# Kernel tuning notes

Measured on AMD Instinct MI355X. Metric: run time of the kernel, lower is better.

## Reference

```python
import jax, jax.numpy as jnp
import numpy as np

HEADS = 8
GROUPS = 8
EPS = 1e-5

def setup_inputs() -> dict:
    key = jax.random.key(0)
    ks = jax.random.split(key, 12)
    B, C, S = 2, 256, 16
    x = jax.random.normal(ks[0], (B, C, S, S, S), dtype=jnp.float32)
    std = 1.0 / np.sqrt(C)
    def lin(k):
        kw, kb = jax.random.split(k)
        W = jax.random.uniform(kw, (C, C), jnp.float32, -std, std)
        b = jax.random.uniform(kb, (C,), jnp.float32, -std, std)
        return W, b
    Wq, bq = lin(ks[1])
    Wk, bk = lin(ks[2])
    Wv, bv = lin(ks[3])
    Wo, bo = lin(ks[4])
    gamma = jnp.ones((C,), jnp.float32)
    beta = jnp.zeros((C,), jnp.float32)
    return {"x": x, "gamma": gamma, "beta": beta, "Wq": Wq, "bq": bq,
            "Wk": Wk, "bk": bk, "Wv": Wv, "bv": bv, "Wo": Wo, "bo": bo}

def _group_norm(x, gamma, beta):
    B, C = x.shape[0], x.shape[1]
    xg = x.reshape(B, GROUPS, -1)  # [B, G, (C/G)*D*H*W]
    mu = xg.mean(axis=-1, keepdims=True)
    var = xg.var(axis=-1, keepdims=True)
    xg = (xg - mu) * jax.lax.rsqrt(var + EPS)
    xn = xg.reshape(x.shape)
    return xn * gamma[None, :, None, None, None] + beta[None, :, None, None, None]

def _conv1x1(x, W, b):
    # 1x1x1 Conv3d == channel-mixing linear: [B,C,D,H,W] x [O,C]
    return jnp.einsum('bcdhw,oc->bodhw', x, W) + b[None, :, None, None, None]

def reference(x, gamma, beta, Wq, bq, Wk, bk, Wv, bv, Wo, bo):
    B, C, D, H, W = x.shape
    hd = C // HEADS
    N = D * H * W
    xn = _group_norm(x, gamma, beta)
    Q = _conv1x1(xn, Wq, bq).reshape(B, HEADS, hd, N)
    K = _conv1x1(xn, Wk, bk).reshape(B, HEADS, hd, N)
    V = _conv1x1(xn, Wv, bv).reshape(B, HEADS, hd, N)
    scale = jnp.sqrt(jnp.asarray(hd, x.dtype))
    attn = jnp.einsum('bhdn,bhdm->bhnm', Q, K) / scale
    attn = jax.nn.softmax(attn, axis=-1)
    out = jnp.einsum('bhnm,bhdm->bhdn', attn, V).reshape(B, C, D, H, W)
    out = _conv1x1(out, Wo, bo)
    return x + out
```

## Files before the change

### kernel.cpp

```cpp
#include <hip/hip_runtime.h>

typedef unsigned short us;
typedef unsigned int uns;
typedef __attribute__((ext_vector_type(8))) short short8;
typedef __attribute__((ext_vector_type(4))) float floatx4;
typedef __attribute__((ext_vector_type(16))) float floatx16;
typedef __attribute__((ext_vector_type(4))) uns unsx4;

__device__ __forceinline__ us f2b(float f) {
    union { float f; unsigned u; } x; x.f = f;
    unsigned r = x.u + 0x7fffu + ((x.u >> 16) & 1u);
    return (us)(r >> 16);
}
__device__ __forceinline__ uns fbits(float f) {
    union { float f; unsigned u; } x; x.f = f; return x.u;
}
__device__ __forceinline__ uns pk2(float hi, float lo) {
    return __builtin_amdgcn_perm(fbits(hi) + 0x8000u, fbits(lo) + 0x8000u, 0x07060302u);
}
__device__ __forceinline__ uns pk2t(float hi, float lo) {
    return __builtin_amdgcn_perm(fbits(hi), fbits(lo), 0x07060302u);
}
__device__ __forceinline__ float ex2(float x) {
    return __builtin_amdgcn_exp2f(x);
}

#define C_DIM 256
#define N_DIM 4096
#define CN (C_DIM * N_DIM)
#define CSC (0.17677669529663687f * 1.4426950408889634f)

__global__ __launch_bounds__(256) void k_part_prep(
        const float* __restrict__ x, float* __restrict__ part,
        const float* __restrict__ Wq, const float* __restrict__ Wk,
        const float* __restrict__ Wv, const float* __restrict__ Wo,
        const float* __restrict__ bq, const float* __restrict__ bk,
        const float* __restrict__ bv, const float* __restrict__ bo,
        us* __restrict__ Wb, float* __restrict__ bst) {
    const int t = threadIdx.x;
    if (blockIdx.y == 16) {
        const int xb = blockIdx.x;
#pragma unroll
        for (int e = 0; e < 4; ++e) {
            int id = e * 16384 + xb * 256 + t;
            Wb[id]          = f2b(Wq[id] * CSC);
            Wb[65536 + id]  = f2b(Wk[id]);
            Wb[131072 + id] = f2b(Wv[id]);
            Wb[196608 + id] = f2b(Wo[id]);
        }
        if (xb == 0) {
            bst[t]       = bq[t] * CSC;
            bst[256 + t] = bk[t];
            bst[512 + t] = bv[t];
            bst[768 + t] = bo[t];
        }
        return;
    }
    const int bg = blockIdx.y, sl = blockIdx.x;
    const float* base = x + (size_t)bg * 131072 + (size_t)sl * 2048 + t * 8;
    float4 a = *(const float4*)base;
    float4 b = *(const float4*)(base + 4);
    float s  = a.x + a.y + a.z + a.w + b.x + b.y + b.z + b.w;
    float ss = a.x*a.x + a.y*a.y + a.z*a.z + a.w*a.w
             + b.x*b.x + b.y*b.y + b.z*b.z + b.w*b.w;
    __shared__ float r1[256], r2[256];
    r1[t] = s; r2[t] = ss;
    __syncthreads();
    for (int off = 128; off > 0; off >>= 1) {
        if (t < off) { r1[t] += r1[t + off]; r2[t] += r2[t + off]; }
        __syncthreads();
    }
    if (t == 0) {
        part[(bg * 64 + sl) * 2]     = r1[0];
        part[(bg * 64 + sl) * 2 + 1] = r2[0];
    }
}

__global__ __launch_bounds__(256) void k_gn_normT(const float* __restrict__ x,
                                                  const float* __restrict__ gamma,
                                                  const float* __restrict__ beta,
                                                  const float* __restrict__ part,
                                                  us* __restrict__ XT) {
    const int t = threadIdx.x, g = blockIdx.y, z = blockIdx.z;
    const int nb = blockIdx.x & 15, c8 = blockIdx.x >> 4;
    const int bg = z * 8 + g;
    __shared__ float scs[32], offs[32], mv[2];
    if (t < 64) {
        float s  = part[(bg * 64 + t) * 2];
        float ss = part[(bg * 64 + t) * 2 + 1];
#pragma unroll
        for (int off = 1; off < 64; off <<= 1) {
            s  += __shfl_xor(s, off, 64);
            ss += __shfl_xor(ss, off, 64);
        }
        if (t == 0) {
            const float inv = 1.f / 131072.f;
            float mean = s * inv;
            float var  = ss * inv - mean * mean;
            mv[0] = mean; mv[1] = rsqrtf(var + 1e-5f);
        }
    }
    __syncthreads();
    if (t < 32) {
        float sc = mv[1] * gamma[g * 32 + t];
        scs[t]  = sc;
        offs[t] = beta[g * 32 + t] - mv[0] * sc;
    }
    __syncthreads();
    const int n = nb * 256 + t;
    const float* xp = x + ((size_t)z * 256 + g * 32) * N_DIM + n;
    us* op = XT + ((size_t)z * N_DIM + n) * 256 + g * 32;
    short8 o;
#pragma unroll
    for (int i = 0; i < 8; ++i) {
        int c = c8 * 8 + i;
        float v = xp[(size_t)c * N_DIM];
        o[i] = (short)f2b(v * scs[c] + offs[c]);
    }
    *(short8*)(op + c8 * 8) = o;
}

__global__ __launch_bounds__(256) void k_qkv(const us* __restrict__ W,
                                             const float* __restrict__ bias,
                                             const us* __restrict__ XT,
                                             us* __restrict__ QT,
                                             us* __restrict__ KTg,
                                             us* __restrict__ Vb) {
    const int t = threadIdx.x;
    const int n0 = blockIdx.x * 64, m0 = blockIdx.y * 64, z = blockIdx.z;
    const int l = t & 63, w = t >> 6, l15 = l & 15, quad = l >> 4;
    const int wm = m0 + (w >> 1) * 32, wn = n0 + (w & 1) * 32;
    const us* Ap = W + (size_t)(wm + l15) * 256 + quad * 8;
    const us* Bp = XT + ((size_t)z * N_DIM + wn + l15) * 256 + quad * 8;

    floatx4 acc[2][2] = {};
#pragma unroll
    for (int k0 = 0; k0 < 256; k0 += 32) {
        short8 a0 = *(const short8*)(Ap + k0);
        short8 a1 = *(const short8*)(Ap + k0 + 16 * 256);
        short8 b0 = *(const short8*)(Bp + k0);
        short8 b1 = *(const short8*)(Bp + k0 + 16 * 256);
        acc[0][0] = __builtin_amdgcn_mfma_f32_16x16x32_bf16(a0, b0, acc[0][0], 0, 0, 0);
        acc[0][1] = __builtin_amdgcn_mfma_f32_16x16x32_bf16(a0, b1, acc[0][1], 0, 0, 0);
        acc[1][0] = __builtin_amdgcn_mfma_f32_16x16x32_bf16(a1, b0, acc[1][0], 0, 0, 0);
        acc[1][1] = __builtin_amdgcn_mfma_f32_16x16x32_bf16(a1, b1, acc[1][1], 0, 0, 0);
    }

    if (blockIdx.y < 8) {
        us* Dst = (blockIdx.y < 4) ? QT : KTg;
        const int h = (wm >> 5) & 7, bh = z * 8 + h;
#pragma unroll
        for (int mt = 0; mt < 2; ++mt) {
            const int d0 = mt * 16 + quad * 4;
            float b0v = bias[wm + mt * 16 + quad * 4 + 0];
            float b1v = bias[wm + mt * 16 + quad * 4 + 1];
            float b2v = bias[wm + mt * 16 + quad * 4 + 2];
            float b3v = bias[wm + mt * 16 + quad * 4 + 3];
#pragma unroll
            for (int nt = 0; nt < 2; ++nt) {
                int col = wn + nt * 16 + l15;
                uint2 pw;
                pw.x = pk2(acc[mt][nt][1] + b1v, acc[mt][nt][0] + b0v);
                pw.y = pk2(acc[mt][nt][3] + b3v, acc[mt][nt][2] + b2v);
                *(uint2*)(Dst + ((size_t)bh * N_DIM + col) * 32 + d0) = pw;
            }
        }
    } else {
#pragma unroll
        for (int mt = 0; mt < 2; ++mt)
#pragma unroll
            for (int nt = 0; nt < 2; ++nt)
#pragma unroll
                for (int r = 0; r < 4; ++r) {
                    int row = wm + mt * 16 + quad * 4 + r;
                    int col = wn + nt * 16 + l15;
                    Vb[((size_t)z * 256 + (row - 512)) * N_DIM + col] =
                        f2b(acc[mt][nt][r] + bias[row]);
                }
    }
}

__device__ __forceinline__ floatx16 mfma32(short8 a, short8 b, floatx16 c) {
    return __builtin_amdgcn_mfma_f32_32x32x16_bf16(a, b, c, 0, 0, 0);
}
__device__ __forceinline__ void mkfrag(const floatx16& s, short8& p1, short8& p2) {
    uns d0 = pk2t(ex2(s[1]),  ex2(s[0]));
    uns d1 = pk2t(ex2(s[3]),  ex2(s[2]));
    uns d2 = pk2t(ex2(s[5]),  ex2(s[4]));
    uns d3 = pk2t(ex2(s[7]),  ex2(s[6]));
    uns d4 = pk2t(ex2(s[9]),  ex2(s[8]));
    uns d5 = pk2t(ex2(s[11]), ex2(s[10]));
    uns d6 = pk2t(ex2(s[13]), ex2(s[12]));
    uns d7 = pk2t(ex2(s[15]), ex2(s[14]));
    asm volatile("v_permlane32_swap_b32 %0, %1" : "+v"(d0), "+v"(d2));
    asm volatile("v_permlane32_swap_b32 %0, %1" : "+v"(d1), "+v"(d3));
    asm volatile("v_permlane32_swap_b32 %0, %1" : "+v"(d4), "+v"(d6));
    asm volatile("v_permlane32_swap_b32 %0, %1" : "+v"(d5), "+v"(d7));
    unsx4 u1 = {d0, d1, d2, d3};
    unsx4 u2 = {d4, d5, d6, d7};
    p1 = __builtin_bit_cast(short8, u1);
    p2 = __builtin_bit_cast(short8, u2);
}

__global__ __launch_bounds__(512, 4) void k_attn(const us* __restrict__ QT,
                                                 const us* __restrict__ KTg,
                                                 const us* __restrict__ Vb,
                                                 us* __restrict__ AOT) {
    __shared__ __attribute__((aligned(16))) us SM[16384];
    us* Kbase = SM;
    us* Vbase = SM + 8192;
    const int t = threadIdx.x;
    const int l = t & 63, w = t >> 6, hf = l >> 5, k31 = l & 31;
    const int sw = w & 3, kh = w >> 2;
    const int bh = blockIdx.y, z = bh >> 3, hd = bh & 7;
    const us* KTp = KTg + (size_t)bh * N_DIM * 32;
    const us* Vp  = Vb  + ((size_t)z * 256 + hd * 32) * N_DIM;
    const int q0 = blockIdx.x * 128 + sw * 32;

    const us* qb = QT + ((size_t)bh * N_DIM + q0 + k31) * 32 + hf * 8;
    short8 bq1 = *(const short8*)qb;
    short8 bq2 = *(const short8*)(qb + 16);
    short8 ones;
#pragma unroll
    for (int j = 0; j < 8; ++j) ones[j] = (short)0x3F80;

    floatx16 o  = (floatx16)0.0f;
    floatx16 dn = (floatx16)0.0f;

    const int krow = sw * 16 + (l >> 2), kslot = l & 3;
    const int kxs  = kslot ^ ((l >> 3) & 3);
    const us* kgs  = KTp + (size_t)(kh * 2048 + krow) * 32 + kslot * 8;
    us*       kds  = Kbase + kh * 2048 + krow * 32 + kxs * 8;
    const int vrow = sw * 8 + (l >> 3), vslot = l & 7;
    const int vxs  = vslot ^ ((l >> 3) & 7);
    const us* vgs  = Vp + (size_t)vrow * N_DIM + kh * 2048 + vslot * 8;
    us*       vds  = Vbase + kh * 2048 + vrow * 64 + vxs * 8;

    const int kf = (k31 >> 1) & 3;
    const us* ka0p = Kbase + kh * 2048 + k31 * 32 + ((hf)     ^ kf) * 8;
    const us* ka1p = Kbase + kh * 2048 + k31 * 32 + ((2 + hf) ^ kf) * 8;
    const int vf = k31 & 7;
    const us* vp0 = Vbase + kh * 2048 + k31 * 64 + ((0 + hf) ^ vf) * 8;
    const us* vp1 = Vbase + kh * 2048 + k31 * 64 + ((2 + hf) ^ vf) * 8;
    const us* vp2 = Vbase + kh * 2048 + k31 * 64 + ((4 + hf) ^ vf) * 8;
    const us* vp3 = Vbase + kh * 2048 + k31 * 64 + ((6 + hf) ^ vf) * 8;

    {
        int4 gk = *(const int4*)kgs;
        int4 gv = *(const int4*)vgs;
        *(int4*)kds = gk;
        *(int4*)vds = gv;
    }
    __syncthreads();
    int cur = 0;

    for (int m0 = 0; m0 < 2048; m0 += 64) {
        const int mnext = (m0 + 64) & 2047;
        int4 ngk = *(const int4*)(kgs + (size_t)mnext * 32);
        int4 ngv = *(const int4*)(vgs + mnext);

        const int bo = cur * 4096;
        short8 ka0 = *(const short8*)(ka0p + bo);
        short8 ka1 = *(const short8*)(ka1p + bo);
        short8 kb0 = *(const short8*)(ka0p + bo + 1024);
        short8 kb1 = *(const short8*)(ka1p + bo + 1024);
        short8 v0  = *(const short8*)(vp0 + bo);
        short8 v1  = *(const short8*)(vp1 + bo);
        short8 v2  = *(const short8*)(vp2 + bo);
        short8 v3  = *(const short8*)(vp3 + bo);

        floatx16 s0 = (floatx16)0.0f, s1 = (floatx16)0.0f;
        s0 = mfma32(ka0, bq1, s0);
        s0 = mfma32(ka1, bq2, s0);
        s1 = mfma32(kb0, bq1, s1);
        s1 = mfma32(kb1, bq2, s1);

        short8 p1, p2, p3, p4;
        mkfrag(s0, p1, p2);
        mkfrag(s1, p3, p4);

        o  = mfma32(v0, p1, o);   dn = mfma32(ones, p1, dn);
        o  = mfma32(v1, p2, o);   dn = mfma32(ones, p2, dn);
        o  = mfma32(v2, p3, o);   dn = mfma32(ones, p3, dn);
        o  = mfma32(v3, p4, o);   dn = mfma32(ones, p4, dn);

        *(int4*)(kds + (cur ^ 1) * 4096) = ngk;
        *(int4*)(vds + (cur ^ 1) * 4096) = ngv;
        __syncthreads();
        cur ^= 1;
    }

    float* sc = (float*)SM;
    if (kh) {
        float* dst = sc + (size_t)(sw * 64 + l) * 20;
        *(floatx4*)(dst + 0)  = ((const floatx4*)&o)[0];
        *(floatx4*)(dst + 4)  = ((const floatx4*)&o)[1];
        *(floatx4*)(dst + 8)  = ((const floatx4*)&o)[2];
        *(floatx4*)(dst + 12) = ((const floatx4*)&o)[3];
        dst[16] = dn[0];
    }
    __syncthreads();
    if (!kh) {
        const float* src = sc + (size_t)(sw * 64 + l) * 20;
        floatx4 a0 = *(const floatx4*)(src + 0);
        floatx4 a1 = *(const floatx4*)(src + 4);
        floatx4 a2 = *(const floatx4*)(src + 8);
        floatx4 a3 = *(const floatx4*)(src + 12);
        const float dtot = dn[0] + src[16];

        float ov[16];
#pragma unroll
        for (int i = 0; i < 4; ++i) {
            ov[i]      = o[i]      + a0[i];
            ov[4 + i]  = o[4 + i]  + a1[i];
            ov[8 + i]  = o[8 + i]  + a2[i];
            ov[12 + i] = o[12 + i] + a3[i];
        }

        const float inv = 1.f / dtot;
        const int q = q0 + k31;
        us* op = AOT + ((size_t)z * N_DIM + q) * 256 + hd * 32 + hf * 4;
#pragma unroll
        for (int g = 0; g < 4; ++g) {
            uint2 u;
            u.x = pk2(ov[4 * g + 1] * inv, ov[4 * g + 0] * inv);
            u.y = pk2(ov[4 * g + 3] * inv, ov[4 * g + 2] * inv);
            *(uint2*)(op + 8 * g) = u;
        }
    }
}

__global__ __launch_bounds__(256) void k_out(const us* __restrict__ W,
                                             const float* __restrict__ bias,
                                             const us* __restrict__ AOT,
                                             float* __restrict__ Out,
                                             const float* __restrict__ resid) {
    const int t = threadIdx.x;
    const int n0 = blockIdx.x * 64, m0 = blockIdx.y * 64, z = blockIdx.z;
    const int l = t & 63, w = t >> 6, l15 = l & 15, quad = l >> 4;
    const int wm = m0 + (w >> 1) * 32, wn = n0 + (w & 1) * 32;
    const us* Ap = W + (size_t)(wm + l15) * 256 + quad * 8;
    const us* Bp = AOT + ((size_t)z * N_DIM + wn + l15) * 256 + quad * 8;

    floatx4 acc[2][2] = {};
#pragma unroll
    for (int k0 = 0; k0 < 256; k0 += 32) {
        short8 a0 = *(const short8*)(Ap + k0);
        short8 a1 = *(const short8*)(Ap + k0 + 16 * 256);
        short8 b0 = *(const short8*)(Bp + k0);
        short8 b1 = *(const short8*)(Bp + k0 + 16 * 256);
        acc[0][0] = __builtin_amdgcn_mfma_f32_16x16x32_bf16(a0, b0, acc[0][0], 0, 0, 0);
        acc[0][1] = __builtin_amdgcn_mfma_f32_16x16x32_bf16(a0, b1, acc[0][1], 0, 0, 0);
        acc[1][0] = __builtin_amdgcn_mfma_f32_16x16x32_bf16(a1, b0, acc[1][0], 0, 0, 0);
        acc[1][1] = __builtin_amdgcn_mfma_f32_16x16x32_bf16(a1, b1, acc[1][1], 0, 0, 0);
    }

#pragma unroll
    for (int mt = 0; mt < 2; ++mt)
#pragma unroll
        for (int nt = 0; nt < 2; ++nt)
#pragma unroll
            for (int r = 0; r < 4; ++r) {
                int row = wm + mt * 16 + quad * 4 + r;
                int col = wn + nt * 16 + l15;
                size_t oidx = ((size_t)z * 256 + row) * N_DIM + col;
                Out[oidx] = acc[mt][nt][r] + bias[row] + resid[oidx];
            }
}

extern "C" void kernel_launch(void* const* d_in, const int* in_sizes, int n_in,
                              void* d_out, int out_size, void* d_ws, size_t ws_size,
                              hipStream_t stream) {
    (void)in_sizes; (void)n_in; (void)out_size; (void)ws_size;
    const float* x     = (const float*)d_in[0];
    const float* gamma = (const float*)d_in[1];
    const float* beta  = (const float*)d_in[2];
    const float* Wq = (const float*)d_in[3]; const float* bq = (const float*)d_in[4];
    const float* Wk = (const float*)d_in[5]; const float* bk = (const float*)d_in[6];
    const float* Wv = (const float*)d_in[7]; const float* bv = (const float*)d_in[8];
    const float* Wo = (const float*)d_in[9]; const float* bo = (const float*)d_in[10];

    float* part = (float*)d_ws;
    us*    Wb   = (us*)((char*)d_ws + 16384);
    float* bst  = (float*)((char*)d_ws + 16384 + 524288);
    us*    XT   = (us*)((char*)d_ws + 16384 + 524288 + 4096);
    us*    QT   = XT + 2 * CN;
    us*    AOT  = QT + 2 * CN;
    us*    Vb   = (us*)d_out;
    us*    KTg  = (us*)d_out + 2 * CN;

    k_part_prep<<<dim3(64, 17), dim3(256), 0, stream>>>(x, part, Wq, Wk, Wv, Wo,
                                                        bq, bk, bv, bo, Wb, bst);
    k_gn_normT<<<dim3(64, 8, 2), dim3(256), 0, stream>>>(x, gamma, beta, part, XT);
    k_qkv<<<dim3(64, 12, 2), dim3(256), 0, stream>>>(Wb, bst, XT, QT, KTg, Vb);
    k_attn<<<dim3(32, 16), dim3(512), 0, stream>>>(QT, KTg, Vb, AOT);
    k_out<<<dim3(64, 4, 2), dim3(256), 0, stream>>>(Wb + 196608, bst + 768, AOT,
                                                    (float*)d_out, x);
}
```

Measured before the change: 167.6 us.

## Split attention keys across four wave groups and halve output GEMM tile

The attention kernel grows from 512 to 1024 threads, so each block now splits the key dimension four ways instead of two. Each wave group walks 1024 keys instead of 2048. The partial numerators and denominators from the three extra groups are reduced through shared memory at the end. The output projection kernel uses 32-row tiles and launches twice as many blocks. Both changes aim to shorten per-block serial work and fill the GPU better, at the cost of more shared memory, more syncs across a larger block, and possibly lower occupancy.

```diff
diff --git a/kernel.cpp b/kernel.cpp
--- a/kernel.cpp
+++ b/kernel.cpp
@@ -202,13 +202,13 @@
     p2 = __builtin_bit_cast(short8, u2);
 }
 
-__global__ __launch_bounds__(512, 4) void k_attn(const us* __restrict__ QT,
-                                                 const us* __restrict__ KTg,
-                                                 const us* __restrict__ Vb,
-                                                 us* __restrict__ AOT) {
-    __shared__ __attribute__((aligned(16))) us SM[16384];
+__global__ __launch_bounds__(1024, 4) void k_attn(const us* __restrict__ QT,
+                                                  const us* __restrict__ KTg,
+                                                  const us* __restrict__ Vb,
+                                                  us* __restrict__ AOT) {
+    __shared__ __attribute__((aligned(16))) us SM[32768];
     us* Kbase = SM;
-    us* Vbase = SM + 8192;
+    us* Vbase = SM + 16384;
     const int t = threadIdx.x;
     const int l = t & 63, w = t >> 6, hf = l >> 5, k31 = l & 31;
     const int sw = w & 3, kh = w >> 2;
@@ -229,11 +229,11 @@
 
     const int krow = sw * 16 + (l >> 2), kslot = l & 3;
     const int kxs  = kslot ^ ((l >> 3) & 3);
-    const us* kgs  = KTp + (size_t)(kh * 2048 + krow) * 32 + kslot * 8;
+    const us* kgs  = KTp + (size_t)(kh * 1024 + krow) * 32 + kslot * 8;
     us*       kds  = Kbase + kh * 2048 + krow * 32 + kxs * 8;
     const int vrow = sw * 8 + (l >> 3), vslot = l & 7;
     const int vxs  = vslot ^ ((l >> 3) & 7);
-    const us* vgs  = Vp + (size_t)vrow * N_DIM + kh * 2048 + vslot * 8;
+    const us* vgs  = Vp + (size_t)vrow * N_DIM + kh * 1024 + vslot * 8;
     us*       vds  = Vbase + kh * 2048 + vrow * 64 + vxs * 8;
 
     const int kf = (k31 >> 1) & 3;
@@ -254,12 +254,12 @@
     __syncthreads();
     int cur = 0;
 
-    for (int m0 = 0; m0 < 2048; m0 += 64) {
-        const int mnext = (m0 + 64) & 2047;
+    for (int m0 = 0; m0 < 1024; m0 += 64) {
+        const int mnext = (m0 + 64) & 1023;
         int4 ngk = *(const int4*)(kgs + (size_t)mnext * 32);
         int4 ngv = *(const int4*)(vgs + mnext);
 
-        const int bo = cur * 4096;
+        const int bo = cur * 8192;
         short8 ka0 = *(const short8*)(ka0p + bo);
         short8 ka1 = *(const short8*)(ka1p + bo);
         short8 kb0 = *(const short8*)(ka0p + bo + 1024);
@@ -284,15 +284,15 @@
         o  = mfma32(v2, p3, o);   dn = mfma32(ones, p3, dn);
         o  = mfma32(v3, p4, o);   dn = mfma32(ones, p4, dn);
 
-        *(int4*)(kds + (cur ^ 1) * 4096) = ngk;
-        *(int4*)(vds + (cur ^ 1) * 4096) = ngv;
+        *(int4*)(kds + (cur ^ 1) * 8192) = ngk;
+        *(int4*)(vds + (cur ^ 1) * 8192) = ngv;
         __syncthreads();
         cur ^= 1;
     }
 
     float* sc = (float*)SM;
     if (kh) {
-        float* dst = sc + (size_t)(sw * 64 + l) * 20;
+        float* dst = sc + (size_t)((kh - 1) * 256 + sw * 64 + l) * 20;
         *(floatx4*)(dst + 0)  = ((const floatx4*)&o)[0];
         *(floatx4*)(dst + 4)  = ((const floatx4*)&o)[1];
         *(floatx4*)(dst + 8)  = ((const floatx4*)&o)[2];
@@ -300,21 +300,26 @@
         dst[16] = dn[0];
     }
     __syncthreads();
-    if (!kh) {
-        const float* src = sc + (size_t)(sw * 64 + l) * 20;
-        floatx4 a0 = *(const floatx4*)(src + 0);
-        floatx4 a1 = *(const floatx4*)(src + 4);
-        floatx4 a2 = *(const floatx4*)(src + 8);
-        floatx4 a3 = *(const floatx4*)(src + 12);
-        const float dtot = dn[0] + src[16];
-
+    if (kh == 0) {
+        float dtot = dn[0];
         float ov[16];
 #pragma unroll
-        for (int i = 0; i < 4; ++i) {
-            ov[i]      = o[i]      + a0[i];
-            ov[4 + i]  = o[4 + i]  + a1[i];
-            ov[8 + i]  = o[8 + i]  + a2[i];
-            ov[12 + i] = o[12 + i] + a3[i];
+        for (int i = 0; i < 16; ++i) ov[i] = o[i];
+#pragma unroll
+        for (int s = 0; s < 3; ++s) {
+            const float* src = sc + (size_t)(s * 256 + sw * 64 + l) * 20;
+            floatx4 a0 = *(const floatx4*)(src + 0);
+            floatx4 a1 = *(const floatx4*)(src + 4);
+            floatx4 a2 = *(const floatx4*)(src + 8);
+            floatx4 a3 = *(const floatx4*)(src + 12);
+#pragma unroll
+            for (int i = 0; i < 4; ++i) {
+                ov[i]      += a0[i];
+                ov[4 + i]  += a1[i];
+                ov[8 + i]  += a2[i];
+                ov[12 + i] += a3[i];
+            }
+            dtot += src[16];
         }
 
         const float inv = 1.f / dtot;
@@ -336,36 +341,31 @@
                                              float* __restrict__ Out,
                                              const float* __restrict__ resid) {
     const int t = threadIdx.x;
-    const int n0 = blockIdx.x * 64, m0 = blockIdx.y * 64, z = blockIdx.z;
+    const int n0 = blockIdx.x * 64, m0 = blockIdx.y * 32, z = blockIdx.z;
     const int l = t & 63, w = t >> 6, l15 = l & 15, quad = l >> 4;
-    const int wm = m0 + (w >> 1) * 32, wn = n0 + (w & 1) * 32;
+    const int wm = m0 + (w >> 1) * 16, wn = n0 + (w & 1) * 32;
     const us* Ap = W + (size_t)(wm + l15) * 256 + quad * 8;
     const us* Bp = AOT + ((size_t)z * N_DIM + wn + l15) * 256 + quad * 8;
 
-    floatx4 acc[2][2] = {};
+    floatx4 acc[2] = {};
 #pragma unroll
     for (int k0 = 0; k0 < 256; k0 += 32) {
         short8 a0 = *(const short8*)(Ap + k0);
-        short8 a1 = *(const short8*)(Ap + k0 + 16 * 256);
         short8 b0 = *(const short8*)(Bp + k0);
         short8 b1 = *(const short8*)(Bp + k0 + 16 * 256);
-        acc[0][0] = __builtin_amdgcn_mfma_f32_16x16x32_bf16(a0, b0, acc[0][0], 0, 0, 0);
-        acc[0][1] = __builtin_amdgcn_mfma_f32_16x16x32_bf16(a0, b1, acc[0][1], 0, 0, 0);
-        acc[1][0] = __builtin_amdgcn_mfma_f32_16x16x32_bf16(a1, b0, acc[1][0], 0, 0, 0);
-        acc[1][1] = __builtin_amdgcn_mfma_f32_16x16x32_bf16(a1, b1, acc[1][1], 0, 0, 0);
-    }
-
-#pragma unroll
-    for (int mt = 0; mt < 2; ++mt)
-#pragma unroll
-        for (int nt = 0; nt < 2; ++nt)
-#pragma unroll
-            for (int r = 0; r < 4; ++r) {
-                int row = wm + mt * 16 + quad * 4 + r;
-                int col = wn + nt * 16 + l15;
-                size_t oidx = ((size_t)z * 256 + row) * N_DIM + col;
-                Out[oidx] = acc[mt][nt][r] + bias[row] + resid[oidx];
-            }
+        acc[0] = __builtin_amdgcn_mfma_f32_16x16x32_bf16(a0, b0, acc[0], 0, 0, 0);
+        acc[1] = __builtin_amdgcn_mfma_f32_16x16x32_bf16(a0, b1, acc[1], 0, 0, 0);
+    }
+
+#pragma unroll
+    for (int nt = 0; nt < 2; ++nt)
+#pragma unroll
+        for (int r = 0; r < 4; ++r) {
+            int row = wm + quad * 4 + r;
+            int col = wn + nt * 16 + l15;
+            size_t oidx = ((size_t)z * 256 + row) * N_DIM + col;
+            Out[oidx] = acc[nt][r] + bias[row] + resid[oidx];
+        }
 }
 
 extern "C" void kernel_launch(void* const* d_in, const int* in_sizes, int n_in,
@@ -393,7 +393,7 @@
                                                         bq, bk, bv, bo, Wb, bst);
     k_gn_normT<<<dim3(64, 8, 2), dim3(256), 0, stream>>>(x, gamma, beta, part, XT);
     k_qkv<<<dim3(64, 12, 2), dim3(256), 0, stream>>>(Wb, bst, XT, QT, KTg, Vb);
-    k_attn<<<dim3(32, 16), dim3(512), 0, stream>>>(QT, KTg, Vb, AOT);
-    k_out<<<dim3(64, 4, 2), dim3(256), 0, stream>>>(Wb + 196608, bst + 768, AOT,
+    k_attn<<<dim3(32, 16), dim3(1024), 0, stream>>>(QT, KTg, Vb, AOT);
+    k_out<<<dim3(64, 8, 2), dim3(256), 0, stream>>>(Wb + 196608, bst + 768, AOT,
                                                     (float*)d_out, x);
 }
```

Measured after the change: 173.4 us. 1.03x slower.
